# Kernel optimization log

Hardware: AMD Instinct MI355X
Metric: run time of the kernel (lower is better)

The kernel has to match this reference:

```python
import jax, jax.numpy as jnp
import numpy as np

NUM_HEADS = 12


def setup_inputs() -> dict:
    key = jax.random.key(0)
    k1, k2, k3 = jax.random.split(key, 3)
    B, N, C = 4, 2048, 768
    x = jax.random.normal(k1, (B, N, C), dtype=jnp.float32)
    # Linear weights stored as [in, out] so y = x @ W (+ b); matches torch Linear math.
    w_qkv = jax.random.normal(k2, (C, 3 * C), dtype=jnp.float32) * (C ** -0.5)
    w_proj = jax.random.normal(k3, (C, C), dtype=jnp.float32) * (C ** -0.5)
    b_proj = jnp.zeros((C,), dtype=jnp.float32)
    return {"x": x, "w_qkv": w_qkv, "w_proj": w_proj, "b_proj": b_proj}


def reference(x, w_qkv, w_proj, b_proj):
    B, N, C = x.shape
    H = NUM_HEADS
    D = C // H
    scale = D ** -0.5
    qkv = (x @ w_qkv).reshape(B, N, 3, H, D)
    qkv = jnp.transpose(qkv, (2, 0, 3, 1, 4))  # [3, B, H, N, D]
    q, k, v = qkv[0], qkv[1], qkv[2]
    attn = jnp.einsum("bhnd,bhmd->bhnm", q, k) * scale  # [B, H, N, N]
    # causal mask (triu with offset 1), filled with -finfo.max as in the torch code
    causal_mask = jnp.triu(jnp.ones((N, N), dtype=bool), k=1)
    mask_value = -jnp.finfo(attn.dtype).max
    attn = jnp.where(causal_mask, mask_value, attn)
    attn = jax.nn.softmax(attn, axis=-1)
    attn = jnp.nan_to_num(attn)
    out = jnp.einsum("bhnm,bhmd->bhnd", attn, v)  # [B, H, N, D]
    out = jnp.transpose(out, (0, 2, 1, 3)).reshape(B, N, C)
    return out @ w_proj + b_proj
```

## Files before the change

### kernel.cpp

```cpp
#include <hip/hip_runtime.h>
#include <hip/hip_bf16.h>
#include <math.h>

#define BATCH 4
#define SEQ   2048
#define CDIM  768
#define NHEAD 12
#define HDIM  64
#define MROWS (BATCH*SEQ)
#define QKVC  (3*CDIM)

typedef __bf16    bf16x8 __attribute__((ext_vector_type(8)));
typedef _Float16  f16x8  __attribute__((ext_vector_type(8)));
typedef _Float16  f16x4  __attribute__((ext_vector_type(4)));
typedef float     f32x4  __attribute__((ext_vector_type(4)));

__device__ __forceinline__ void async16(const void* g, void* l) {
  __builtin_amdgcn_global_load_lds(
      (const __attribute__((address_space(1))) void*)g,
      (__attribute__((address_space(3))) void*)l, 16, 0, 0);
}

__global__ __launch_bounds__(256) void cast_f32_bf16(
    const float* __restrict__ in, __bf16* __restrict__ out, int n8) {
  int i = blockIdx.x * 256 + threadIdx.x;
  if (i >= n8) return;
  float4 a = reinterpret_cast<const float4*>(in)[i * 2];
  float4 b = reinterpret_cast<const float4*>(in)[i * 2 + 1];
  bf16x8 o;
  o[0] = (__bf16)a.x; o[1] = (__bf16)a.y; o[2] = (__bf16)a.z; o[3] = (__bf16)a.w;
  o[4] = (__bf16)b.x; o[5] = (__bf16)b.y; o[6] = (__bf16)b.z; o[7] = (__bf16)b.w;
  reinterpret_cast<bf16x8*>(out)[i] = o;
}

__global__ __launch_bounds__(256) void transpose_cast(
    const float* __restrict__ w, __bf16* __restrict__ wt, int K, int N) {
  __shared__ float sh[32][33];
  const int n0 = blockIdx.x * 32, k0 = blockIdx.y * 32;
  const int tx = threadIdx.x, ty = threadIdx.y;
#pragma unroll
  for (int i = 0; i < 4; ++i)
    sh[ty + i * 8][tx] = w[(size_t)(k0 + ty + i * 8) * N + n0 + tx];
  __syncthreads();
#pragma unroll
  for (int i = 0; i < 4; ++i)
    wt[(size_t)(n0 + ty + i * 8) * K + k0 + tx] = (__bf16)sh[tx][ty + i * 8];
}

template <bool BF16OUT>
__global__ __launch_bounds__(256) void gemm_bf16_kernel(
    const __bf16* __restrict__ A, const __bf16* __restrict__ Bt,
    const float* __restrict__ bias, void* __restrict__ Cout,
    int M, int N, int K) {
  __shared__ __align__(16) __bf16 As[128 * 32];
  __shared__ __align__(16) __bf16 Bs[128 * 32];
  const int tid  = threadIdx.x;
  const int w    = tid >> 6;
  const int lane = tid & 63;
  const int quad = lane >> 4;
  const int lr   = lane & 15;
  const int wr   = w >> 1, wc = w & 1;
  const int mBase = blockIdx.y * 128, nBase = blockIdx.x * 128;

  f32x4 acc[4][4] = {};

  const int srow = lane >> 2;
  const int sk8  = (lane & 3) * 8;
  const __bf16* aSrc0 = A  + (size_t)(mBase + w * 32 + srow) * K + sk8;
  const __bf16* aSrc1 = aSrc0 + (size_t)16 * K;
  const __bf16* bSrc0 = Bt + (size_t)(nBase + w * 32 + srow) * K + sk8;
  const __bf16* bSrc1 = bSrc0 + (size_t)16 * K;
  __bf16* aDst0 = &As[(w * 32 + 0) * 32];
  __bf16* aDst1 = &As[(w * 32 + 16) * 32];
  __bf16* bDst0 = &Bs[(w * 32 + 0) * 32];
  __bf16* bDst1 = &Bs[(w * 32 + 16) * 32];

  for (int k0 = 0; k0 < K; k0 += 32) {
    __syncthreads();
    async16(aSrc0 + k0, aDst0);
    async16(aSrc1 + k0, aDst1);
    async16(bSrc0 + k0, bDst0);
    async16(bSrc1 + k0, bDst1);
    __syncthreads();

    bf16x8 af[4], bfr[4];
#pragma unroll
    for (int mt = 0; mt < 4; ++mt)
      af[mt] = *reinterpret_cast<const bf16x8*>(
          &As[(wr * 64 + mt * 16 + lr) * 32 + quad * 8]);
#pragma unroll
    for (int nt = 0; nt < 4; ++nt)
      bfr[nt] = *reinterpret_cast<const bf16x8*>(
          &Bs[(wc * 64 + nt * 16 + lr) * 32 + quad * 8]);
#pragma unroll
    for (int mt = 0; mt < 4; ++mt)
#pragma unroll
      for (int nt = 0; nt < 4; ++nt)
        acc[mt][nt] = __builtin_amdgcn_mfma_f32_16x16x32_bf16(
            af[mt], bfr[nt], acc[mt][nt], 0, 0, 0);
  }

#pragma unroll
  for (int mt = 0; mt < 4; ++mt) {
#pragma unroll
    for (int nt = 0; nt < 4; ++nt) {
      const int col = nBase + wc * 64 + nt * 16 + lr;
#pragma unroll
      for (int r = 0; r < 4; ++r) {
        const size_t row = (size_t)(mBase + wr * 64 + mt * 16 + quad * 4 + r);
        if (BF16OUT) {
          ((__bf16*)Cout)[row * N + col] = (__bf16)acc[mt][nt][r];
        } else {
          ((float*)Cout)[row * N + col] = acc[mt][nt][r] + bias[col];
        }
      }
    }
  }
}

__global__ __launch_bounds__(256) void swizzle_kv(
    const __bf16* __restrict__ qkv, __bf16* __restrict__ kF,
    _Float16* __restrict__ vF) {
  const int kt = blockIdx.x;
  const int hb = blockIdx.y;
  const int h = hb % NHEAD, b = hb / NHEAD;
  const int tid = threadIdx.x;

  __shared__ __align__(16) __bf16 Ksh[64][72];
  __shared__ __align__(16) _Float16 Vsh[64][72];

  const int sr = tid >> 3;
  const int sc = (tid & 7) * 8;
  const __bf16* kbase = qkv + (size_t)(b * SEQ + kt * 64) * QKVC + CDIM + h * HDIM;
  const __bf16* vbase = kbase + CDIM;

#pragma unroll
  for (int rr = 0; rr < 2; ++rr) {
    const int row = sr + rr * 32;
    bf16x8 kv = *reinterpret_cast<const bf16x8*>(kbase + (size_t)row * QKVC + sc);
    *reinterpret_cast<bf16x8*>(&Ksh[row][sc]) = kv;
    bf16x8 vv = *reinterpret_cast<const bf16x8*>(vbase + (size_t)row * QKVC + sc);
    f16x8 vf;
#pragma unroll
    for (int j = 0; j < 8; ++j) vf[j] = (_Float16)(float)vv[j];
    *reinterpret_cast<f16x8*>(&Vsh[row][sc]) = vf;
  }
  __syncthreads();

  const size_t tileOff = ((size_t)(hb * 32 + kt)) * 4096;

#pragma unroll
  for (int ss = 0; ss < 2; ++ss) {
    const int s = tid + ss * 256;
    const int f = s >> 6, lane = s & 63;
    const int nt = f >> 1, kc = f & 1;
    const int lq = lane >> 4, ll = lane & 15;
    bf16x8 frag = *reinterpret_cast<const bf16x8*>(
        &Ksh[nt * 16 + ll][kc * 32 + lq * 8]);
    *reinterpret_cast<bf16x8*>(&kF[tileOff + (size_t)f * 512 + lane * 8]) = frag;
  }
#pragma unroll
  for (int ss = 0; ss < 2; ++ss) {
    const int s = tid + ss * 256;
    const int g = s >> 6, lane = s & 63;
    const int nt = g >> 1, ph = g & 1;
    const int lq = lane >> 4, ll = lane & 15;
    f16x8 frag;
#pragma unroll
    for (int j = 0; j < 8; ++j)
      frag[j] = Vsh[nt * 16 + lq * 4 + (j & 3)][(ph * 2 + (j >> 2)) * 16 + ll];
    *reinterpret_cast<f16x8*>(&vF[tileOff + (size_t)g * 512 + lane * 8]) = frag;
  }
}

__global__ __launch_bounds__(256, 2) void flash_mfma_kernel(
    const __bf16* __restrict__ qkv, const __bf16* __restrict__ kF,
    const _Float16* __restrict__ vF, __bf16* __restrict__ out) {
  const int bid  = blockIdx.x;
  const int tid  = threadIdx.x;
  const int w    = tid >> 6;
  const int lane = tid & 63;
  const int quad = lane >> 4;
  const int lr   = lane & 15;

  const int x   = bid & 7;
  const int i   = bid >> 3;
  const int hb  = x * 6 + (i >> 3);
  const int qt  = 31 - ((i & 7) * 4 + w);
  const int h   = hb % NHEAD, b = hb / NHEAD;

  bf16x8 qf[4][2];
  {
    const float qs = 0.125f * 1.44269504088896f;
    const __bf16* qp = qkv + (size_t)(b * SEQ + qt * 64) * QKVC + h * HDIM;
#pragma unroll
    for (int qg = 0; qg < 4; ++qg)
#pragma unroll
      for (int kc = 0; kc < 2; ++kc) {
        bf16x8 qr = *reinterpret_cast<const bf16x8*>(
            qp + (size_t)(qg * 16 + lr) * QKVC + kc * 32 + quad * 8);
        bf16x8 f;
#pragma unroll
        for (int j = 0; j < 8; ++j) f[j] = (__bf16)((float)qr[j] * qs);
        qf[qg][kc] = f;
      }
  }

  f32x4 O[4][4] = {};
  f32x4 O4[4] = {};

  const __bf16*   kT = kF + ((size_t)(hb * 32)) * 4096 + lane * 8;
  const _Float16* vT = vF + ((size_t)(hb * 32)) * 4096 + lane * 8;
  const f16x4 vones = {(_Float16)1.f, (_Float16)1.f, (_Float16)1.f, (_Float16)1.f};

  for (int kt = 0; kt <= qt; ++kt) {
    bf16x8 kf[8];
    f16x8  vf8[8];
#pragma unroll
    for (int f = 0; f < 8; ++f)
      kf[f] = *reinterpret_cast<const bf16x8*>(kT + (size_t)kt * 4096 + f * 512);
#pragma unroll
    for (int g = 0; g < 8; ++g)
      vf8[g] = *reinterpret_cast<const f16x8*>(vT + (size_t)kt * 4096 + g * 512);

#pragma unroll
    for (int nt = 0; nt < 4; ++nt) {
      f32x4 s[4];
#pragma unroll
      for (int qg = 0; qg < 4; ++qg) {
        f32x4 acc = (f32x4){0.f, 0.f, 0.f, 0.f};
        acc = __builtin_amdgcn_mfma_f32_16x16x32_bf16(kf[nt * 2 + 0], qf[qg][0], acc, 0, 0, 0);
        acc = __builtin_amdgcn_mfma_f32_16x16x32_bf16(kf[nt * 2 + 1], qf[qg][1], acc, 0, 0, 0);
        s[qg] = acc;
      }
      if (kt == qt) {
#pragma unroll
        for (int qg = 0; qg < 4; ++qg)
#pragma unroll
          for (int r = 0; r < 4; ++r)
            if (nt * 16 + quad * 4 + r > qg * 16 + lr) s[qg][r] = -1e30f;
      }
      f16x4 pa[4];
#pragma unroll
      for (int qg = 0; qg < 4; ++qg) {
        f16x4 t;
#pragma unroll
        for (int r = 0; r < 4; ++r)
          t[r] = (_Float16)__builtin_amdgcn_exp2f(s[qg][r]);
        pa[qg] = t;
      }
#pragma unroll
      for (int qg = 0; qg < 4; ++qg)
        O4[qg] = __builtin_amdgcn_mfma_f32_16x16x16f16(pa[qg], vones, O4[qg], 0, 0, 0);
#pragma unroll
      for (int dt = 0; dt < 4; ++dt) {
        const f16x8 vv = vf8[nt * 2 + (dt >> 1)];
        f16x4 vb;
#pragma unroll
        for (int j = 0; j < 4; ++j) vb[j] = vv[(dt & 1) * 4 + j];
#pragma unroll
        for (int qg = 0; qg < 4; ++qg)
          O[qg][dt] = __builtin_amdgcn_mfma_f32_16x16x16f16(pa[qg], vb, O[qg][dt], 0, 0, 0);
      }
    }
  }

  __bf16* obase = out + (size_t)(b * SEQ + qt * 64) * CDIM + h * HDIM;
#pragma unroll
  for (int qg = 0; qg < 4; ++qg) {
    float linv[4];
#pragma unroll
    for (int r = 0; r < 4; ++r) linv[r] = 1.f / O4[qg][r];
#pragma unroll
    for (int dt = 0; dt < 4; ++dt)
#pragma unroll
      for (int r = 0; r < 4; ++r)
        obase[(size_t)(qg * 16 + quad * 4 + r) * CDIM + dt * 16 + lr] =
            (__bf16)(O[qg][dt][r] * linv[r]);
  }
}

extern "C" void kernel_launch(void* const* d_in, const int* in_sizes, int n_in,
                              void* d_out, int out_size, void* d_ws, size_t ws_size,
                              hipStream_t stream) {
  const float* x      = (const float*)d_in[0];
  const float* w_qkv  = (const float*)d_in[1];
  const float* w_proj = (const float*)d_in[2];
  const float* b_proj = (const float*)d_in[3];
  float* out = (float*)d_out;

  __bf16* qkv    = (__bf16*)d_ws;
  __bf16* attnb  = qkv + (size_t)MROWS * QKVC;
  __bf16* xb     = attnb + (size_t)MROWS * CDIM;
  __bf16* wqkvT  = xb + (size_t)MROWS * CDIM;
  __bf16* wprojT = wqkvT + (size_t)QKVC * CDIM;
  __bf16* kFb    = wprojT + (size_t)CDIM * CDIM;
  _Float16* vFb  = (_Float16*)(kFb + (size_t)48 * 32 * 4096);

  cast_f32_bf16<<<dim3((MROWS * CDIM / 8 + 255) / 256), dim3(256), 0, stream>>>(
      x, xb, MROWS * CDIM / 8);
  transpose_cast<<<dim3(QKVC / 32, CDIM / 32), dim3(32, 8), 0, stream>>>(
      w_qkv, wqkvT, CDIM, QKVC);
  transpose_cast<<<dim3(CDIM / 32, CDIM / 32), dim3(32, 8), 0, stream>>>(
      w_proj, wprojT, CDIM, CDIM);

  gemm_bf16_kernel<true><<<dim3(QKVC / 128, MROWS / 128), dim3(256), 0, stream>>>(
      xb, wqkvT, nullptr, qkv, MROWS, QKVC, CDIM);

  swizzle_kv<<<dim3(32, 48), dim3(256), 0, stream>>>(qkv, kFb, vFb);

  flash_mfma_kernel<<<dim3(384), dim3(256), 0, stream>>>(qkv, kFb, vFb, attnb);

  gemm_bf16_kernel<false><<<dim3(CDIM / 128, MROWS / 128), dim3(256), 0, stream>>>(
      attnb, wprojT, b_proj, out, MROWS, CDIM, CDIM);
}
```

Baseline: 239.8 us.

## Split KV loop across waves per query tile with LDS reduction

The flash attention kernel now assigns one 64-row query tile per block and strides the KV tiles across its four waves, instead of giving each wave its own query tile. Partial O accumulators and row sums are combined through shared memory in a two-step tree reduction before one wave normalizes and writes the output. This quadruples the grid and evens out the causal work imbalance across waves and CUs. The occupancy hint rises to three blocks per CU, which adds register pressure and possible spills, plus the cost of extra barriers and LDS traffic.

```diff
diff --git a/kernel.cpp b/kernel.cpp
--- a/kernel.cpp
+++ b/kernel.cpp
@@ -173,7 +173,7 @@
   }
 }
 
-__global__ __launch_bounds__(256, 2) void flash_mfma_kernel(
+__global__ __launch_bounds__(256, 3) void flash_mfma_kernel(
     const __bf16* __restrict__ qkv, const __bf16* __restrict__ kF,
     const _Float16* __restrict__ vF, __bf16* __restrict__ out) {
   const int bid  = blockIdx.x;
@@ -184,10 +184,12 @@
   const int lr   = lane & 15;
 
   const int x   = bid & 7;
-  const int i   = bid >> 3;
-  const int hb  = x * 6 + (i >> 3);
-  const int qt  = 31 - ((i & 7) * 4 + w);
+  const int g   = bid >> 3;
+  const int qt  = 31 - (g / 6);
+  const int hb  = x * 6 + (g % 6);
   const int h   = hb % NHEAD, b = hb / NHEAD;
+
+  __shared__ __align__(16) float Red[2][64 * 80];
 
   bf16x8 qf[4][2];
   {
@@ -213,15 +215,15 @@
   const _Float16* vT = vF + ((size_t)(hb * 32)) * 4096 + lane * 8;
   const f16x4 vones = {(_Float16)1.f, (_Float16)1.f, (_Float16)1.f, (_Float16)1.f};
 
-  for (int kt = 0; kt <= qt; ++kt) {
+  for (int kt = w; kt <= qt; kt += 4) {
     bf16x8 kf[8];
     f16x8  vf8[8];
 #pragma unroll
     for (int f = 0; f < 8; ++f)
       kf[f] = *reinterpret_cast<const bf16x8*>(kT + (size_t)kt * 4096 + f * 512);
 #pragma unroll
-    for (int g = 0; g < 8; ++g)
-      vf8[g] = *reinterpret_cast<const f16x8*>(vT + (size_t)kt * 4096 + g * 512);
+    for (int gg = 0; gg < 8; ++gg)
+      vf8[gg] = *reinterpret_cast<const f16x8*>(vT + (size_t)kt * 4096 + gg * 512);
 
 #pragma unroll
     for (int nt = 0; nt < 4; ++nt) {
@@ -265,18 +267,66 @@
     }
   }
 
-  __bf16* obase = out + (size_t)(b * SEQ + qt * 64) * CDIM + h * HDIM;
-#pragma unroll
-  for (int qg = 0; qg < 4; ++qg) {
-    float linv[4];
-#pragma unroll
-    for (int r = 0; r < 4; ++r) linv[r] = 1.f / O4[qg][r];
-#pragma unroll
-    for (int dt = 0; dt < 4; ++dt)
-#pragma unroll
-      for (int r = 0; r < 4; ++r)
-        obase[(size_t)(qg * 16 + quad * 4 + r) * CDIM + dt * 16 + lr] =
-            (__bf16)(O[qg][dt][r] * linv[r]);
+  if (w == 1 || w == 3) {
+    float* dst = Red[w >> 1];
+#pragma unroll
+    for (int qg = 0; qg < 4; ++qg)
+#pragma unroll
+      for (int dt = 0; dt < 4; ++dt)
+        *reinterpret_cast<f32x4*>(&dst[((qg * 4 + dt) * 64 + lane) * 4]) = O[qg][dt];
+#pragma unroll
+    for (int qg = 0; qg < 4; ++qg)
+      *reinterpret_cast<f32x4*>(&dst[((16 + qg) * 64 + lane) * 4]) = O4[qg];
+  }
+  __syncthreads();
+  if (w == 0 || w == 2) {
+    const float* src = Red[w >> 1];
+#pragma unroll
+    for (int qg = 0; qg < 4; ++qg)
+#pragma unroll
+      for (int dt = 0; dt < 4; ++dt)
+        O[qg][dt] += *reinterpret_cast<const f32x4*>(&src[((qg * 4 + dt) * 64 + lane) * 4]);
+#pragma unroll
+    for (int qg = 0; qg < 4; ++qg)
+      O4[qg] += *reinterpret_cast<const f32x4*>(&src[((16 + qg) * 64 + lane) * 4]);
+  }
+  __syncthreads();
+  if (w == 2) {
+    float* dst = Red[0];
+#pragma unroll
+    for (int qg = 0; qg < 4; ++qg)
+#pragma unroll
+      for (int dt = 0; dt < 4; ++dt)
+        *reinterpret_cast<f32x4*>(&dst[((qg * 4 + dt) * 64 + lane) * 4]) = O[qg][dt];
+#pragma unroll
+    for (int qg = 0; qg < 4; ++qg)
+      *reinterpret_cast<f32x4*>(&dst[((16 + qg) * 64 + lane) * 4]) = O4[qg];
+  }
+  __syncthreads();
+  if (w == 0) {
+    const float* src = Red[0];
+#pragma unroll
+    for (int qg = 0; qg < 4; ++qg)
+#pragma unroll
+      for (int dt = 0; dt < 4; ++dt)
+        O[qg][dt] += *reinterpret_cast<const f32x4*>(&src[((qg * 4 + dt) * 64 + lane) * 4]);
+#pragma unroll
+    for (int qg = 0; qg < 4; ++qg)
+      O4[qg] += *reinterpret_cast<const f32x4*>(&src[((16 + qg) * 64 + lane) * 4]);
+
+    __bf16* obase = out + (size_t)(b * SEQ + qt * 64) * CDIM + h * HDIM;
+#pragma unroll
+    for (int qg = 0; qg < 4; ++qg) {
+      float linv[4];
+#pragma unroll
+      for (int r = 0; r < 4; ++r) linv[r] = 1.f / O4[qg][r];
+#pragma unroll
+      for (int dt = 0; dt < 4; ++dt)
+#pragma unroll
+        for (int r = 0; r < 4; ++r)
+          obase[(size_t)(qg * 16 + quad * 4 + r) * CDIM + dt * 16 + lr] =
+              (__bf16)(O[qg][dt][r] * linv[r]);
+    }
   }
 }
 
@@ -309,7 +359,7 @@
 
   swizzle_kv<<<dim3(32, 48), dim3(256), 0, stream>>>(qkv, kFb, vFb);
 
-  flash_mfma_kernel<<<dim3(384), dim3(256), 0, stream>>>(qkv, kFb, vFb, attnb);
+  flash_mfma_kernel<<<dim3(1536), dim3(256), 0, stream>>>(qkv, kFb, vFb, attnb);
 
   gemm_bf16_kernel<false><<<dim3(CDIM / 128, MROWS / 128), dim3(256), 0, stream>>>(
       attnb, wprojT, b_proj, out, MROWS, CDIM, CDIM);
```

After: 247.6 us. +3.3%, slower.
